# Kernel optimization log

Measured on AMD Instinct MI355X. Metric: run time of the kernel, lower is better.

## Reference

```python
import jax, jax.numpy as jnp
import numpy as np

DIM = 512
NUM_LATENTS = 128
TRUE_BATCH = 8
DOWNSCALING = 16


def setup_inputs() -> dict:
    key = jax.random.key(0)
    ks = jax.random.split(key, 7)
    B = TRUE_BATCH * NUM_LATENTS
    s = 0.02
    return {
        "x": jax.random.normal(ks[0], (B, DOWNSCALING, DIM), dtype=jnp.float32),
        "l": jax.random.normal(ks[1], (B, NUM_LATENTS, DIM), dtype=jnp.float32),
        "Wq": jax.random.normal(ks[2], (DIM, DIM), dtype=jnp.float32) * s,
        "Wk": jax.random.normal(ks[3], (DIM, DIM), dtype=jnp.float32) * s,
        "Wv": jax.random.normal(ks[4], (DIM, DIM), dtype=jnp.float32) * s,
        "Wo": jax.random.normal(ks[5], (DIM, DIM), dtype=jnp.float32) * s,
        "bo": jax.random.normal(ks[6], (DIM,), dtype=jnp.float32) * s,
        "num_heads": 8,
    }


def reference(x, l, Wq, Wk, Wv, Wo, bo, num_heads):
    B, n_tok, d = x.shape
    num_latents = l.shape[1]
    dh = d // num_heads

    def split_heads(t):
        # (b, n, h*d) -> (b, h, n, d)
        b, n, _ = t.shape
        return t.reshape(b, n, num_heads, dh).transpose(0, 2, 1, 3)

    q = split_heads(x @ Wq.T)   # (B, h, n_tok, dh)
    k = split_heads(l @ Wk.T)   # (B, h, num_latents, dh)
    v = split_heads(l @ Wv.T)

    scores = jnp.einsum('bhid,bhjd->bhij', q, k) * (dh ** -0.5)

    # mask row for batch element b is row (b mod num_latents) of a causal triu mask:
    # latent index m may attend only to latents j <= m.
    row = jnp.arange(B) % num_latents                       # (B,)
    allowed = jnp.arange(num_latents)[None, :] <= row[:, None]  # (B, num_latents)
    mask = jnp.where(allowed, 0.0, -jnp.inf).astype(scores.dtype)

    scores = scores + mask[:, None, None, :]
    attn = jax.nn.softmax(scores, axis=-1)

    out = jnp.einsum('bhij,bhjd->bhid', attn, v)            # (B, h, n_tok, dh)
    out = out.transpose(0, 2, 1, 3).reshape(B, n_tok, d)
    return out @ Wo.T + bo
```

## Files before the change

### kernel.cpp

```cpp
#include <hip/hip_runtime.h>


typedef __bf16 bf16;
typedef __attribute__((ext_vector_type(8))) __bf16 bf16x8;
typedef __attribute__((ext_vector_type(4))) __bf16 bf16x4;
typedef __attribute__((ext_vector_type(4))) float  float4v;

#define MFMA16(a, b, c) __builtin_amdgcn_mfma_f32_16x16x32_bf16((a), (b), (c), 0, 0, 0)

__global__ __launch_bounds__(256) void cast_w(const float* __restrict__ src,
                                              bf16* __restrict__ dst) {
    int i = (blockIdx.x * 256 + threadIdx.x) * 4;
    float4v f = *(const float4v*)(src + i);
    bf16x4 o = {(bf16)f.x, (bf16)f.y, (bf16)f.z, (bf16)f.w};
    *(bf16x4*)(dst + i) = o;
}

template <bool AFP32, bool FOUT>
__global__ __launch_bounds__(256) void gemm_bt(const void* __restrict__ Ap,
                                               const bf16* __restrict__ W,
                                               void* __restrict__ Cp,
                                               const float* __restrict__ bias) {
    __shared__ bf16 Asl[128 * 32];
    __shared__ bf16 Bsl[128 * 32];

    const int tid  = threadIdx.x;
    const int n0   = blockIdx.x * 128;
    const int m0   = blockIdx.y * 128;

    const int wave = tid >> 6;
    const int lane = tid & 63;
    const int mi   = lane & 15;
    const int quad = lane >> 4;
    const int qrow = (wave >> 1) * 64;
    const int qcol = (wave & 1) * 64;

    const int sr = tid >> 1;
    const int sc = (tid & 1) * 16;

    float4v acc[4][4] = {};

    for (int kt = 0; kt < 16; ++kt) {
        const int k0 = kt * 32;
        if (AFP32) {
            const float* A = (const float*)Ap + (m0 + sr) * 512 + k0 + sc;
            float4v f0 = ((const float4v*)A)[0];
            float4v f1 = ((const float4v*)A)[1];
            float4v f2 = ((const float4v*)A)[2];
            float4v f3 = ((const float4v*)A)[3];
            bf16* d = &Asl[sr * 32 + sc];
            ((bf16x4*)d)[0] = bf16x4{(bf16)f0.x, (bf16)f0.y, (bf16)f0.z, (bf16)f0.w};
            ((bf16x4*)d)[1] = bf16x4{(bf16)f1.x, (bf16)f1.y, (bf16)f1.z, (bf16)f1.w};
            ((bf16x4*)d)[2] = bf16x4{(bf16)f2.x, (bf16)f2.y, (bf16)f2.z, (bf16)f2.w};
            ((bf16x4*)d)[3] = bf16x4{(bf16)f3.x, (bf16)f3.y, (bf16)f3.z, (bf16)f3.w};
        } else {
            const bf16* A = (const bf16*)Ap + (m0 + sr) * 512 + k0 + sc;
            bf16* d = &Asl[sr * 32 + sc];
            ((bf16x8*)d)[0] = ((const bf16x8*)A)[0];
            ((bf16x8*)d)[1] = ((const bf16x8*)A)[1];
        }
        {
            const bf16* Wp = W + (n0 + sr) * 512 + k0 + sc;
            bf16* d = &Bsl[sr * 32 + sc];
            ((bf16x8*)d)[0] = ((const bf16x8*)Wp)[0];
            ((bf16x8*)d)[1] = ((const bf16x8*)Wp)[1];
        }
        __syncthreads();

        bf16x8 af[4], bfr[4];
#pragma unroll
        for (int i = 0; i < 4; ++i)
            af[i] = *(const bf16x8*)&Asl[(qrow + i * 16 + mi) * 32 + quad * 8];
#pragma unroll
        for (int j = 0; j < 4; ++j)
            bfr[j] = *(const bf16x8*)&Bsl[(qcol + j * 16 + mi) * 32 + quad * 8];
#pragma unroll
        for (int i = 0; i < 4; ++i)
#pragma unroll
            for (int j = 0; j < 4; ++j)
                acc[i][j] = MFMA16(af[i], bfr[j], acc[i][j]);
        __syncthreads();
    }

#pragma unroll
    for (int i = 0; i < 4; ++i) {
#pragma unroll
        for (int j = 0; j < 4; ++j) {
            const int row = m0 + qrow + i * 16 + quad * 4;
            const int col = n0 + qcol + j * 16 + mi;
#pragma unroll
            for (int r = 0; r < 4; ++r) {
                float v = acc[i][j][r];
                if (FOUT)
                    ((float*)Cp)[(row + r) * 512 + col] = v + bias[col];
                else
                    ((bf16*)Cp)[(row + r) * 512 + col] = (bf16)v;
            }
        }
    }
}

__global__ __launch_bounds__(64) void attn_kernel(const bf16* __restrict__ Q,
                                                  const bf16* __restrict__ K,
                                                  const bf16* __restrict__ V,
                                                  bf16* __restrict__ O) {
    __shared__ bf16 Plds[16 * 128];
    __shared__ bf16 Vt[64 * 128];

    const int bh   = blockIdx.x;
    const int b    = bh >> 3;
    const int h    = bh & 7;
    const int rowb = b & 127;
    const int lane = threadIdx.x;
    const int mi   = lane & 15;
    const int quad = lane >> 4;

    const bf16* qbase = Q + (b * 16 + mi) * 512 + h * 64 + quad * 8;
    bf16x8 aq0 = *(const bf16x8*)(qbase);
    bf16x8 aq1 = *(const bf16x8*)(qbase + 32);

    float4v sc[8];
    const bf16* kbase = K + (b * 128 + mi) * 512 + h * 64 + quad * 8;
#pragma unroll
    for (int jt = 0; jt < 8; ++jt) {
        const bf16* kb = kbase + jt * 16 * 512;
        bf16x8 bk0 = *(const bf16x8*)(kb);
        bf16x8 bk1 = *(const bf16x8*)(kb + 32);
        float4v a = {};
        a = MFMA16(aq0, bk0, a);
        a = MFMA16(aq1, bk1, a);
        sc[jt] = a;
    }

#pragma unroll
    for (int jt = 0; jt < 8; ++jt) {
        const bool masked = (jt * 16 + mi) > rowb;
#pragma unroll
        for (int r = 0; r < 4; ++r)
            sc[jt][r] = masked ? -1e30f : sc[jt][r] * 0.125f;
    }

#pragma unroll
    for (int r = 0; r < 4; ++r) {
        float mx = sc[0][r];
#pragma unroll
        for (int jt = 1; jt < 8; ++jt) mx = fmaxf(mx, sc[jt][r]);
#pragma unroll
        for (int off = 1; off < 16; off <<= 1) mx = fmaxf(mx, __shfl_xor(mx, off, 64));
        float s = 0.f;
#pragma unroll
        for (int jt = 0; jt < 8; ++jt) {
            float p = __expf(sc[jt][r] - mx);
            sc[jt][r] = p;
            s += p;
        }
#pragma unroll
        for (int off = 1; off < 16; off <<= 1) s += __shfl_xor(s, off, 64);
        const float inv = 1.f / s;
#pragma unroll
        for (int jt = 0; jt < 8; ++jt)
            Plds[(quad * 4 + r) * 128 + jt * 16 + mi] = (bf16)(sc[jt][r] * inv);
    }

    const int vr = lane >> 3;
    const int vc = lane & 7;
#pragma unroll
    for (int p = 0; p < 16; ++p) {
        const int lat = p * 8 + vr;
        bf16x8 v8 = *(const bf16x8*)(V + (b * 128 + lat) * 512 + h * 64 + vc * 8);
#pragma unroll
        for (int e = 0; e < 8; ++e) Vt[(vc * 8 + e) * 128 + lat] = v8[e];
    }
    __syncthreads();

    float4v ao[4] = {};
#pragma unroll
    for (int ks = 0; ks < 4; ++ks) {
        bf16x8 ap = *(const bf16x8*)&Plds[mi * 128 + ks * 32 + quad * 8];
#pragma unroll
        for (int jt = 0; jt < 4; ++jt) {
            bf16x8 bv = *(const bf16x8*)&Vt[(jt * 16 + mi) * 128 + ks * 32 + quad * 8];
            ao[jt] = MFMA16(ap, bv, ao[jt]);
        }
    }

#pragma unroll
    for (int jt = 0; jt < 4; ++jt)
#pragma unroll
        for (int r = 0; r < 4; ++r)
            O[(b * 16 + quad * 4 + r) * 512 + h * 64 + jt * 16 + mi] = (bf16)ao[jt][r];
}

extern "C" void kernel_launch(void* const* d_in, const int* in_sizes, int n_in,
                              void* d_out, int out_size, void* d_ws, size_t ws_size,
                              hipStream_t stream) {
    const float* x  = (const float*)d_in[0];
    const float* l  = (const float*)d_in[1];
    const float* Wq = (const float*)d_in[2];
    const float* Wk = (const float*)d_in[3];
    const float* Wv = (const float*)d_in[4];
    const float* Wo = (const float*)d_in[5];
    const float* bo = (const float*)d_in[6];

    char* ws = (char*)d_ws;
    const size_t WSZ = 512 * 512 * 2;
    bf16* Wq_b = (bf16*)(ws + 0 * WSZ);
    bf16* Wk_b = (bf16*)(ws + 1 * WSZ);
    bf16* Wv_b = (bf16*)(ws + 2 * WSZ);
    bf16* Wo_b = (bf16*)(ws + 3 * WSZ);
    size_t off = 4 * WSZ;
    bf16* Qb  = (bf16*)(ws + off); off += (size_t)16384 * 512 * 2;
    bf16* Kb  = (bf16*)(ws + off); off += (size_t)131072 * 512 * 2;
    bf16* Vb  = (bf16*)(ws + off); off += (size_t)131072 * 512 * 2;
    bf16* AOb = (bf16*)(ws + off);

    cast_w<<<256, 256, 0, stream>>>(Wq, Wq_b);
    cast_w<<<256, 256, 0, stream>>>(Wk, Wk_b);
    cast_w<<<256, 256, 0, stream>>>(Wv, Wv_b);
    cast_w<<<256, 256, 0, stream>>>(Wo, Wo_b);

    gemm_bt<true, false><<<dim3(4, 128),  256, 0, stream>>>(x, Wq_b, Qb, nullptr);
    gemm_bt<true, false><<<dim3(4, 1024), 256, 0, stream>>>(l, Wk_b, Kb, nullptr);
    gemm_bt<true, false><<<dim3(4, 1024), 256, 0, stream>>>(l, Wv_b, Vb, nullptr);

    attn_kernel<<<8192, 64, 0, stream>>>(Qb, Kb, Vb, AOb);

    gemm_bt<false, true><<<dim3(4, 128), 256, 0, stream>>>(AOb, Wo_b, d_out, bo);
}
```

Baseline: 825.5 us.

## Fuse K/V projection, pre-cast inputs, use direct-to-LDS loads, skip masked attention tiles

Weights are cast in one fused kernel, and x and l are pre-cast to bf16 in separate passes. The K and V projections become one GEMM over a concatenated weight, so l is read once. The GEMM now loads A and B tiles with global_load_lds straight into shared memory. The attention kernel skips key tiles that the causal mask fully excludes and reads V directly from global memory instead of transposing it through LDS. The extra cast pass adds a full read and write of l, and the strided per-element V loads may coalesce poorly.

Result: faster. 730.3 us (-11.5%).

```diff
diff --git a/kernel.cpp b/kernel.cpp
--- a/kernel.cpp
+++ b/kernel.cpp
@@ -8,21 +8,48 @@
 
 #define MFMA16(a, b, c) __builtin_amdgcn_mfma_f32_16x16x32_bf16((a), (b), (c), 0, 0, 0)
 
-__global__ __launch_bounds__(256) void cast_w(const float* __restrict__ src,
-                                              bf16* __restrict__ dst) {
-    int i = (blockIdx.x * 256 + threadIdx.x) * 4;
-    float4v f = *(const float4v*)(src + i);
-    bf16x4 o = {(bf16)f.x, (bf16)f.y, (bf16)f.z, (bf16)f.w};
-    *(bf16x4*)(dst + i) = o;
-}
-
-template <bool AFP32, bool FOUT>
-__global__ __launch_bounds__(256) void gemm_bt(const void* __restrict__ Ap,
+__device__ __forceinline__ void gl2lds16(const bf16* g, bf16* l) {
+    __builtin_amdgcn_global_load_lds(
+        (const __attribute__((address_space(1))) void*)g,
+        (__attribute__((address_space(3))) void*)l, 16, 0, 0);
+}
+
+__global__ __launch_bounds__(256) void cast_f32_bf16(const float* __restrict__ src,
+                                                     bf16* __restrict__ dst, int n4) {
+    const int stride = gridDim.x * 256;
+    for (int i = blockIdx.x * 256 + threadIdx.x; i < n4; i += stride) {
+        float4v f = ((const float4v*)src)[i];
+        ((bf16x4*)dst)[i] = bf16x4{(bf16)f.x, (bf16)f.y, (bf16)f.z, (bf16)f.w};
+    }
+}
+
+__global__ __launch_bounds__(256) void cast_weights(const float* __restrict__ Wq,
+                                                    const float* __restrict__ Wk,
+                                                    const float* __restrict__ Wv,
+                                                    const float* __restrict__ Wo,
+                                                    bf16* __restrict__ Wq_b,
+                                                    bf16* __restrict__ Wkv_b,
+                                                    bf16* __restrict__ Wo_b) {
+    const int i = blockIdx.x * 256 + threadIdx.x;
+    const int w = i >> 16;
+    const int j = i & 65535;
+    const float* src = (w == 0) ? Wq : (w == 1) ? Wk : (w == 2) ? Wv : Wo;
+    bf16x4* dst = (w == 0) ? (bf16x4*)Wq_b
+                : (w == 1) ? (bf16x4*)Wkv_b
+                : (w == 2) ? ((bf16x4*)Wkv_b) + 65536
+                           : (bf16x4*)Wo_b;
+    float4v f = ((const float4v*)src)[j];
+    dst[j] = bf16x4{(bf16)f.x, (bf16)f.y, (bf16)f.z, (bf16)f.w};
+}
+
+template <bool FOUT>
+__global__ __launch_bounds__(256) void gemm_bt(const bf16* __restrict__ A,
                                                const bf16* __restrict__ W,
                                                void* __restrict__ Cp,
-                                               const float* __restrict__ bias) {
-    __shared__ bf16 Asl[128 * 32];
-    __shared__ bf16 Bsl[128 * 32];
+                                               const float* __restrict__ bias,
+                                               int ldC) {
+    __shared__ alignas(16) bf16 Asl[128 * 32];
+    __shared__ alignas(16) bf16 Bsl[128 * 32];
 
     const int tid  = threadIdx.x;
     const int n0   = blockIdx.x * 128;
@@ -35,35 +62,19 @@
     const int qrow = (wave >> 1) * 64;
     const int qcol = (wave & 1) * 64;
 
-    const int sr = tid >> 1;
-    const int sc = (tid & 1) * 16;
+    const int srow = wave * 16 + (lane >> 2);
+    const int scol = (lane & 3) * 8;
 
     float4v acc[4][4] = {};
 
     for (int kt = 0; kt < 16; ++kt) {
         const int k0 = kt * 32;
-        if (AFP32) {
-            const float* A = (const float*)Ap + (m0 + sr) * 512 + k0 + sc;
-            float4v f0 = ((const float4v*)A)[0];
-            float4v f1 = ((const float4v*)A)[1];
-            float4v f2 = ((const float4v*)A)[2];
-            float4v f3 = ((const float4v*)A)[3];
-            bf16* d = &Asl[sr * 32 + sc];
-            ((bf16x4*)d)[0] = bf16x4{(bf16)f0.x, (bf16)f0.y, (bf16)f0.z, (bf16)f0.w};
-            ((bf16x4*)d)[1] = bf16x4{(bf16)f1.x, (bf16)f1.y, (bf16)f1.z, (bf16)f1.w};
-            ((bf16x4*)d)[2] = bf16x4{(bf16)f2.x, (bf16)f2.y, (bf16)f2.z, (bf16)f2.w};
-            ((bf16x4*)d)[3] = bf16x4{(bf16)f3.x, (bf16)f3.y, (bf16)f3.z, (bf16)f3.w};
-        } else {
-            const bf16* A = (const bf16*)Ap + (m0 + sr) * 512 + k0 + sc;
-            bf16* d = &Asl[sr * 32 + sc];
-            ((bf16x8*)d)[0] = ((const bf16x8*)A)[0];
-            ((bf16x8*)d)[1] = ((const bf16x8*)A)[1];
-        }
-        {
-            const bf16* Wp = W + (n0 + sr) * 512 + k0 + sc;
-            bf16* d = &Bsl[sr * 32 + sc];
-            ((bf16x8*)d)[0] = ((const bf16x8*)Wp)[0];
-            ((bf16x8*)d)[1] = ((const bf16x8*)Wp)[1];
+#pragma unroll
+        for (int r = 0; r < 2; ++r) {
+            gl2lds16(A + (size_t)(m0 + srow + r * 64) * 512 + k0 + scol,
+                     &Asl[wave * 512 + r * 2048]);
+            gl2lds16(W + (size_t)(n0 + srow + r * 64) * 512 + k0 + scol,
+                     &Bsl[wave * 512 + r * 2048]);
         }
         __syncthreads();
 
@@ -92,95 +103,103 @@
             for (int r = 0; r < 4; ++r) {
                 float v = acc[i][j][r];
                 if (FOUT)
-                    ((float*)Cp)[(row + r) * 512 + col] = v + bias[col];
+                    ((float*)Cp)[(size_t)(row + r) * ldC + col] = v + bias[col];
                 else
-                    ((bf16*)Cp)[(row + r) * 512 + col] = (bf16)v;
+                    ((bf16*)Cp)[(size_t)(row + r) * ldC + col] = (bf16)v;
             }
         }
     }
 }
 
 __global__ __launch_bounds__(64) void attn_kernel(const bf16* __restrict__ Q,
-                                                  const bf16* __restrict__ K,
-                                                  const bf16* __restrict__ V,
+                                                  const bf16* __restrict__ KV,
                                                   bf16* __restrict__ O) {
-    __shared__ bf16 Plds[16 * 128];
-    __shared__ bf16 Vt[64 * 128];
-
-    const int bh   = blockIdx.x;
-    const int b    = bh >> 3;
-    const int h    = bh & 7;
-    const int rowb = b & 127;
-    const int lane = threadIdx.x;
-    const int mi   = lane & 15;
-    const int quad = lane >> 4;
-
-    const bf16* qbase = Q + (b * 16 + mi) * 512 + h * 64 + quad * 8;
-    bf16x8 aq0 = *(const bf16x8*)(qbase);
-    bf16x8 aq1 = *(const bf16x8*)(qbase + 32);
+    __shared__ alignas(16) bf16 Plds[16 * 136];
+
+    const int bh     = blockIdx.x;
+    const int b      = bh >> 3;
+    const int h      = bh & 7;
+    const int rowb   = b & 127;
+    const int ntiles = (rowb >> 4) + 1;
+    const int nkt    = (ntiles + 1) >> 1;
+    const int lane   = threadIdx.x;
+    const int mi     = lane & 15;
+    const int quad   = lane >> 4;
+
+    const bf16* qbase = Q + (size_t)(b * 16 + mi) * 512 + h * 64 + quad * 8;
+    const bf16x8 aq0 = *(const bf16x8*)(qbase);
+    const bf16x8 aq1 = *(const bf16x8*)(qbase + 32);
 
     float4v sc[8];
-    const bf16* kbase = K + (b * 128 + mi) * 512 + h * 64 + quad * 8;
+    const bf16* kbase = KV + (size_t)(b * 128 + mi) * 1024 + h * 64 + quad * 8;
 #pragma unroll
     for (int jt = 0; jt < 8; ++jt) {
-        const bf16* kb = kbase + jt * 16 * 512;
-        bf16x8 bk0 = *(const bf16x8*)(kb);
-        bf16x8 bk1 = *(const bf16x8*)(kb + 32);
-        float4v a = {};
-        a = MFMA16(aq0, bk0, a);
-        a = MFMA16(aq1, bk1, a);
-        sc[jt] = a;
+        if (jt < ntiles) {
+            const bf16* kb = kbase + (size_t)jt * 16 * 1024;
+            bf16x8 bk0 = *(const bf16x8*)(kb);
+            bf16x8 bk1 = *(const bf16x8*)(kb + 32);
+            float4v a = {};
+            a = MFMA16(aq0, bk0, a);
+            a = MFMA16(aq1, bk1, a);
+            sc[jt] = a;
+        }
     }
 
 #pragma unroll
     for (int jt = 0; jt < 8; ++jt) {
-        const bool masked = (jt * 16 + mi) > rowb;
-#pragma unroll
-        for (int r = 0; r < 4; ++r)
-            sc[jt][r] = masked ? -1e30f : sc[jt][r] * 0.125f;
+        if (jt < ntiles) {
+            const bool masked = (jt * 16 + mi) > rowb;
+#pragma unroll
+            for (int r = 0; r < 4; ++r)
+                sc[jt][r] = masked ? -1e30f : sc[jt][r] * 0.125f;
+        }
     }
 
 #pragma unroll
     for (int r = 0; r < 4; ++r) {
         float mx = sc[0][r];
 #pragma unroll
-        for (int jt = 1; jt < 8; ++jt) mx = fmaxf(mx, sc[jt][r]);
+        for (int jt = 1; jt < 8; ++jt)
+            if (jt < ntiles) mx = fmaxf(mx, sc[jt][r]);
 #pragma unroll
         for (int off = 1; off < 16; off <<= 1) mx = fmaxf(mx, __shfl_xor(mx, off, 64));
         float s = 0.f;
 #pragma unroll
         for (int jt = 0; jt < 8; ++jt) {
-            float p = __expf(sc[jt][r] - mx);
-            sc[jt][r] = p;
-            s += p;
+            if (jt < ntiles) {
+                float p = __expf(sc[jt][r] - mx);
+                sc[jt][r] = p;
+                s += p;
+            }
         }
 #pragma unroll
         for (int off = 1; off < 16; off <<= 1) s += __shfl_xor(s, off, 64);
         const float inv = 1.f / s;
 #pragma unroll
-        for (int jt = 0; jt < 8; ++jt)
-            Plds[(quad * 4 + r) * 128 + jt * 16 + mi] = (bf16)(sc[jt][r] * inv);
-    }
-
-    const int vr = lane >> 3;
-    const int vc = lane & 7;
-#pragma unroll
-    for (int p = 0; p < 16; ++p) {
-        const int lat = p * 8 + vr;
-        bf16x8 v8 = *(const bf16x8*)(V + (b * 128 + lat) * 512 + h * 64 + vc * 8);
-#pragma unroll
-        for (int e = 0; e < 8; ++e) Vt[(vc * 8 + e) * 128 + lat] = v8[e];
+        for (int jt = 0; jt < 8; ++jt) {
+            if (jt < 2 * nkt) {
+                float p = (jt < ntiles) ? sc[jt][r] * inv : 0.f;
+                Plds[(quad * 4 + r) * 136 + jt * 16 + mi] = (bf16)p;
+            }
+        }
     }
     __syncthreads();
 
     float4v ao[4] = {};
 #pragma unroll
     for (int ks = 0; ks < 4; ++ks) {
-        bf16x8 ap = *(const bf16x8*)&Plds[mi * 128 + ks * 32 + quad * 8];
-#pragma unroll
-        for (int jt = 0; jt < 4; ++jt) {
-            bf16x8 bv = *(const bf16x8*)&Vt[(jt * 16 + mi) * 128 + ks * 32 + quad * 8];
-            ao[jt] = MFMA16(ap, bv, ao[jt]);
+        if (ks < nkt) {
+            bf16x8 ap = *(const bf16x8*)&Plds[mi * 136 + ks * 32 + quad * 8];
+            const bf16* vbase = KV + (size_t)(b * 128 + ks * 32 + quad * 8) * 1024
+                               + 512 + h * 64;
+#pragma unroll
+            for (int jt = 0; jt < 4; ++jt) {
+                bf16x8 bv;
+#pragma unroll
+                for (int j = 0; j < 8; ++j)
+                    bv[j] = vbase[(size_t)j * 1024 + jt * 16 + mi];
+                ao[jt] = MFMA16(ap, bv, ao[jt]);
+            }
         }
     }
 
@@ -188,7 +207,8 @@
     for (int jt = 0; jt < 4; ++jt)
 #pragma unroll
         for (int r = 0; r < 4; ++r)
-            O[(b * 16 + quad * 4 + r) * 512 + h * 64 + jt * 16 + mi] = (bf16)ao[jt][r];
+            O[(size_t)(b * 16 + quad * 4 + r) * 512 + h * 64 + jt * 16 + mi] =
+                (bf16)ao[jt][r];
 }
 
 extern "C" void kernel_launch(void* const* d_in, const int* in_sizes, int n_in,
@@ -203,27 +223,24 @@
     const float* bo = (const float*)d_in[6];
 
     char* ws = (char*)d_ws;
-    const size_t WSZ = 512 * 512 * 2;
-    bf16* Wq_b = (bf16*)(ws + 0 * WSZ);
-    bf16* Wk_b = (bf16*)(ws + 1 * WSZ);
-    bf16* Wv_b = (bf16*)(ws + 2 * WSZ);
-    bf16* Wo_b = (bf16*)(ws + 3 * WSZ);
-    size_t off = 4 * WSZ;
-    bf16* Qb  = (bf16*)(ws + off); off += (size_t)16384 * 512 * 2;
-    bf16* Kb  = (bf16*)(ws + off); off += (size_t)131072 * 512 * 2;
-    bf16* Vb  = (bf16*)(ws + off); off += (size_t)131072 * 512 * 2;
-    bf16* AOb = (bf16*)(ws + off);
-
-    cast_w<<<256, 256, 0, stream>>>(Wq, Wq_b);
-    cast_w<<<256, 256, 0, stream>>>(Wk, Wk_b);
-    cast_w<<<256, 256, 0, stream>>>(Wv, Wv_b);
-    cast_w<<<256, 256, 0, stream>>>(Wo, Wo_b);
-
-    gemm_bt<true, false><<<dim3(4, 128),  256, 0, stream>>>(x, Wq_b, Qb, nullptr);
-    gemm_bt<true, false><<<dim3(4, 1024), 256, 0, stream>>>(l, Wk_b, Kb, nullptr);
-    gemm_bt<true, false><<<dim3(4, 1024), 256, 0, stream>>>(l, Wv_b, Vb, nullptr);
-
-    attn_kernel<<<8192, 64, 0, stream>>>(Qb, Kb, Vb, AOb);
-
-    gemm_bt<false, true><<<dim3(4, 128), 256, 0, stream>>>(AOb, Wo_b, d_out, bo);
-}
+    size_t off = 0;
+    bf16* Wq_b  = (bf16*)(ws + off); off += (size_t)512 * 512 * 2;
+    bf16* Wo_b  = (bf16*)(ws + off); off += (size_t)512 * 512 * 2;
+    bf16* Wkv_b = (bf16*)(ws + off); off += (size_t)1024 * 512 * 2;
+    bf16* xb    = (bf16*)(ws + off); off += (size_t)16384 * 512 * 2;
+    bf16* lb    = (bf16*)(ws + off); off += (size_t)131072 * 512 * 2;
+    bf16* Qb    = (bf16*)(ws + off); off += (size_t)16384 * 512 * 2;
+    bf16* KVb   = (bf16*)(ws + off); off += (size_t)131072 * 1024 * 2;
+    bf16* AOb   = (bf16*)(ws + off);
+
+    cast_weights<<<1024, 256, 0, stream>>>(Wq, Wk, Wv, Wo, Wq_b, Wkv_b, Wo_b);
+    cast_f32_bf16<<<2048, 256, 0, stream>>>(x, xb, 16384 * 512 / 4);
+    cast_f32_bf16<<<8192, 256, 0, stream>>>(l, lb, 131072 * 512 / 4);
+
+    gemm_bt<false><<<dim3(4, 128),  256, 0, stream>>>(xb, Wq_b,  Qb,  nullptr, 512);
+    gemm_bt<false><<<dim3(8, 1024), 256, 0, stream>>>(lb, Wkv_b, KVb, nullptr, 1024);
+
+    attn_kernel<<<8192, 64, 0, stream>>>(Qb, KVb, AOb);
+
+    gemm_bt<true><<<dim3(4, 128), 256, 0, stream>>>(AOb, Wo_b, d_out, bo, 512);
+}
```
